# Kernel tuning notes

Hardware: AMD Instinct MI355X
Metric: run time of the kernel (lower is better)

Reference implementation:

```python
import jax, jax.numpy as jnp
import numpy as np

D_MODEL = 1024
STATE_DIM = 256


def setup_inputs() -> dict:
    key = jax.random.key(0)
    k_u, k_lam, k_B, k_C = jax.random.split(key, 4)
    u = jax.random.normal(k_u, (4, 4096, D_MODEL), dtype=jnp.float32)
    # log_lambda ~ N(3.0, 0.5^2), matching torch.randn(state_dim)*0.5 + 3.0
    log_lambda = jax.random.normal(k_lam, (STATE_DIM,), dtype=jnp.float32) * 0.5 + 3.0
    # torch Linear weights: B.weight [state_dim, d_model], C.weight [d_model, state_dim]
    B_w = jax.random.normal(k_B, (STATE_DIM, D_MODEL), dtype=jnp.float32) / np.sqrt(D_MODEL)
    C_w = jax.random.normal(k_C, (D_MODEL, STATE_DIM), dtype=jnp.float32) / np.sqrt(STATE_DIM)
    D = jnp.zeros((D_MODEL,), dtype=jnp.float32)
    return {"u": u, "log_lambda": log_lambda, "B_w": B_w, "C_w": C_w, "D": D}


def reference(u, log_lambda, B_w, C_w, D):
    # u: [batch, seq, d_model]
    lam = jax.nn.sigmoid(log_lambda)                      # [state_dim]
    Bu = jnp.einsum('bsd,nd->bsn', u, B_w)                # [batch, seq, state_dim]

    def step(h, bu_t):
        h = lam * h + bu_t                                # [batch, state_dim]
        return h, h

    h0 = jnp.zeros((u.shape[0], lam.shape[0]), dtype=u.dtype)
    # scan over time axis; Bu transposed to [seq, batch, state_dim]
    _, hs = jax.lax.scan(step, h0, jnp.swapaxes(Bu, 0, 1))
    hs = jnp.swapaxes(hs, 0, 1)                           # [batch, seq, state_dim]
    y = jnp.einsum('bsn,dn->bsd', hs, C_w) + D * u        # [batch, seq, d_model]
    return y
```

## Files before the change

### kernel.cpp

```cpp
#include <hip/hip_runtime.h>
#include <math.h>

typedef unsigned short ushort_t;
typedef __bf16 v8bf __attribute__((ext_vector_type(8)));
typedef __bf16 v4bf __attribute__((ext_vector_type(4)));
typedef float  v4f  __attribute__((ext_vector_type(4)));
typedef float  f32x4 __attribute__((ext_vector_type(4)));

#define BATCH 4
#define SEQ 4096
#define DM 1024
#define NS 256
#define MROWS (BATCH*SEQ)

#define NCH 128
#define CL (SEQ/NCH)

#define BK 32

typedef __attribute__((address_space(1))) void as1_void;
typedef __attribute__((address_space(3))) void as3_void;

__device__ __forceinline__ void gl_lds16(const void* g, void* l) {
    __builtin_amdgcn_global_load_lds((as1_void*)g, (as3_void*)l, 16, 0, 0);
}

__device__ __forceinline__ ushort_t f2bf(float f) {
    unsigned u = __builtin_bit_cast(unsigned, f);
    u += 0x7fff + ((u >> 16) & 1);
    return (ushort_t)(u >> 16);
}

__device__ __forceinline__ float sigm(float x) { return 1.0f / (1.0f + expf(-x)); }

__device__ __forceinline__ float powk(int e, float l1, float l2, float l4,
                                      float l8, float l16) {
    float w = 1.0f;
    if (e & 1)  w *= l1;
    if (e & 2)  w *= l2;
    if (e & 4)  w *= l4;
    if (e & 8)  w *= l8;
    if (e & 16) w *= l16;
    return w;
}

__global__ __launch_bounds__(256)
void gemm1_fused(const float* __restrict__ A,
                 const ushort_t* __restrict__ B,
                 float* __restrict__ Bu,
                 const float* __restrict__ ll,
                 float* __restrict__ cf)
{
    const int K = DM;
    __shared__ __align__(16) ushort_t As[2][128*BK];
    __shared__ __align__(16) ushort_t Bs[2][64*BK];

    const int tid  = threadIdx.x;
    const int lane = tid & 63;
    const int wave = tid >> 6;
    const int wrow = wave >> 1;
    const int wcol = wave & 1;
    const int n0 = blockIdx.x * 64;
    const int m0 = blockIdx.y * 128;

    const int fr = lane & 15;
    const int fq = lane >> 4;

    int arow[4], ac4[4];
    #pragma unroll
    for (int j = 0; j < 4; ++j) {
        int cid = j*256 + tid;
        arow[j] = cid >> 3;
        ac4[j]  = (cid & 7) * 4;
    }
    const int brow = tid >> 2;
    const int bcol = (tid & 3) * 8;

    f32x4 acc[4][2] = {};
    v4f areg[4];

    #pragma unroll
    for (int j = 0; j < 4; ++j)
        areg[j] = *(const v4f*)&A[(size_t)(m0 + arow[j])*K + ac4[j]];
    gl_lds16(&B[(size_t)(n0 + brow)*K + bcol], &Bs[0][tid*8]);

    for (int it = 0; it < K/BK; ++it) {
        const int cur = it & 1;
        #pragma unroll
        for (int j = 0; j < 4; ++j)
            *(v4bf*)&As[cur][arow[j]*BK + ac4[j]] = __builtin_convertvector(areg[j], v4bf);
        __syncthreads();

        if (it + 1 < K/BK) {
            const int k1 = (it + 1) * BK;
            gl_lds16(&B[(size_t)(n0 + brow)*K + k1 + bcol], &Bs[cur ^ 1][tid*8]);
            #pragma unroll
            for (int j = 0; j < 4; ++j)
                areg[j] = *(const v4f*)&A[(size_t)(m0 + arow[j])*K + k1 + ac4[j]];
        }

        v8bf af[4], bf[2];
        #pragma unroll
        for (int mi = 0; mi < 4; ++mi)
            af[mi] = *reinterpret_cast<const v8bf*>(&As[cur][(wrow*64 + mi*16 + fr)*BK + fq*8]);
        #pragma unroll
        for (int ni = 0; ni < 2; ++ni)
            bf[ni] = *reinterpret_cast<const v8bf*>(&Bs[cur][(wcol*32 + ni*16 + fr)*BK + fq*8]);

        #pragma unroll
        for (int mi = 0; mi < 4; ++mi)
            #pragma unroll
            for (int ni = 0; ni < 2; ++ni)
                acc[mi][ni] = __builtin_amdgcn_mfma_f32_16x16x32_bf16(
                                  af[mi], bf[ni], acc[mi][ni], 0, 0, 0);
    }

    const int orow = m0 + wrow*64 + (lane >> 4)*4;
    const int ocol = n0 + wcol*32 + (lane & 15);
    #pragma unroll
    for (int mi = 0; mi < 4; ++mi)
        #pragma unroll
        for (int ni = 0; ni < 2; ++ni)
            #pragma unroll
            for (int r = 0; r < 4; ++r)
                Bu[(size_t)(orow + mi*16 + r) * NS + (ocol + ni*16)] = acc[mi][ni][r];

    const int b_idx  = m0 >> 12;
    const int c_base = (m0 & 4095) >> 5;
    const int base   = (lane >> 4) * 4;

    #pragma unroll
    for (int ni = 0; ni < 2; ++ni) {
        const int col = ocol + ni*16;
        const float l1  = sigm(ll[col]);
        const float l2  = l1*l1;
        const float l4  = l2*l2;
        const float l8  = l4*l4;
        const float l16 = l8*l8;
        #pragma unroll
        for (int half = 0; half < 2; ++half) {
            float f = 0.0f;
            #pragma unroll
            for (int mi2 = 0; mi2 < 2; ++mi2) {
                const int mi = half*2 + mi2;
                float w = powk(28 - mi2*16 - base, l1, l2, l4, l8, l16);
                f = fmaf(w, acc[mi][ni][3], f);
                w *= l1; f = fmaf(w, acc[mi][ni][2], f);
                w *= l1; f = fmaf(w, acc[mi][ni][1], f);
                w *= l1; f = fmaf(w, acc[mi][ni][0], f);
            }
            f += __shfl_xor(f, 16, 64);
            f += __shfl_xor(f, 32, 64);
            if ((lane >> 4) == 0) {
                const int chunk = c_base + wrow*2 + half;
                cf[((size_t)b_idx*NCH + chunk)*NS + col] = f;
            }
        }
    }
}

__global__ __launch_bounds__(256)
void gemm2_mfma(const ushort_t* __restrict__ A,
                const ushort_t* __restrict__ B,
                float* __restrict__ C,
                const float* __restrict__ Dvec, const float* __restrict__ U)
{
    const int K = NS;
    const int N = DM;
    __shared__ __align__(16) ushort_t As[2][128*BK];
    __shared__ __align__(16) ushort_t Bs[2][128*BK];

    const int tid  = threadIdx.x;
    const int lane = tid & 63;
    const int wave = tid >> 6;
    const int wrow = wave >> 1;
    const int wcol = wave & 1;
    const int n0 = blockIdx.x * 128;
    const int m0 = blockIdx.y * 128;

    const int fr = lane & 15;
    const int fq = lane >> 4;

    f32x4 acc[4][4] = {};

    const int ch0 = wave*128 + lane;
    const int ch1 = ch0 + 64;
    const int r0 = ch0 >> 2, c0 = (ch0 & 3) * 8;
    const int r1 = ch1 >> 2, c1 = (ch1 & 3) * 8;

    gl_lds16(&A[(size_t)(m0 + r0)*K + c0], &As[0][ch0*8]);
    gl_lds16(&B[(size_t)(n0 + r0)*K + c0], &Bs[0][ch0*8]);
    gl_lds16(&A[(size_t)(m0 + r1)*K + c1], &As[0][ch1*8]);
    gl_lds16(&B[(size_t)(n0 + r1)*K + c1], &Bs[0][ch1*8]);

    for (int it = 0; it < K/BK; ++it) {
        const int cur = it & 1;
        __syncthreads();

        if (it + 1 < K/BK) {
            const int k1 = (it + 1) * BK;
            gl_lds16(&A[(size_t)(m0 + r0)*K + k1 + c0], &As[cur^1][ch0*8]);
            gl_lds16(&B[(size_t)(n0 + r0)*K + k1 + c0], &Bs[cur^1][ch0*8]);
            gl_lds16(&A[(size_t)(m0 + r1)*K + k1 + c1], &As[cur^1][ch1*8]);
            gl_lds16(&B[(size_t)(n0 + r1)*K + k1 + c1], &Bs[cur^1][ch1*8]);
        }

        v8bf af[4], bf[4];
        #pragma unroll
        for (int mi = 0; mi < 4; ++mi)
            af[mi] = *reinterpret_cast<const v8bf*>(&As[cur][(wrow*64 + mi*16 + fr)*BK + fq*8]);
        #pragma unroll
        for (int ni = 0; ni < 4; ++ni)
            bf[ni] = *reinterpret_cast<const v8bf*>(&Bs[cur][(wcol*64 + ni*16 + fr)*BK + fq*8]);

        #pragma unroll
        for (int mi = 0; mi < 4; ++mi)
            #pragma unroll
            for (int ni = 0; ni < 4; ++ni)
                acc[mi][ni] = __builtin_amdgcn_mfma_f32_16x16x32_bf16(
                                  af[mi], bf[ni], acc[mi][ni], 0, 0, 0);
    }

    const int orow = m0 + wrow*64 + (lane >> 4)*4;
    const int ocol = n0 + wcol*64 + (lane & 15);
    #pragma unroll
    for (int ni = 0; ni < 4; ++ni) {
        const int col = ocol + ni*16;
        const float d = Dvec[col];
        #pragma unroll
        for (int mi = 0; mi < 4; ++mi) {
            #pragma unroll
            for (int r = 0; r < 4; ++r) {
                const size_t idx = (size_t)(orow + mi*16 + r) * N + col;
                float v = acc[mi][ni][r];
                if (d != 0.0f) v = fmaf(d, U[idx], v);
                C[idx] = v;
            }
        }
    }
}

__global__ __launch_bounds__(256)
void cvt_w(const float4* __restrict__ Bw, const float4* __restrict__ Cw,
           ushort_t* __restrict__ Bo, ushort_t* __restrict__ Co)
{
    const int i = blockIdx.x * 256 + threadIdx.x;
    const float4* src = blockIdx.y ? Cw : Bw;
    ushort_t*     dst = blockIdx.y ? Co : Bo;
    float4 v = src[i];
    ushort4 o;
    o.x = f2bf(v.x); o.y = f2bf(v.y); o.z = f2bf(v.z); o.w = f2bf(v.w);
    *(ushort4*)&dst[4*(size_t)i] = o;
}

__global__ __launch_bounds__(256)
void carry_scan(const float* __restrict__ ll, const float* __restrict__ cf,
                float* __restrict__ carry)
{
    const int n = threadIdx.x, b = blockIdx.x;
    const float lam = sigm(ll[n]);
    float lamL = lam;
    #pragma unroll
    for (int i = 0; i < 5; ++i) lamL *= lamL;

    const float* cfb = cf    + (size_t)b*NCH*NS + n;
    float*       cab = carry + (size_t)b*NCH*NS + n;

    float x = 0.0f;
    for (int c0 = 0; c0 < NCH; c0 += 16) {
        float v[16];
        #pragma unroll
        for (int j = 0; j < 16; ++j) v[j] = cfb[(size_t)(c0 + j)*NS];
        #pragma unroll
        for (int j = 0; j < 16; ++j) {
            cab[(size_t)(c0 + j)*NS] = x;
            x = fmaf(lamL, x, v[j]);
        }
    }
}

__global__ __launch_bounds__(256)
void scan_apply(const float* __restrict__ Bu, const float* __restrict__ ll,
                const float* __restrict__ carry, ushort_t* __restrict__ hs16)
{
    const int n = threadIdx.x, c = blockIdx.x, b = blockIdx.y;
    const float lam = sigm(ll[n]);
    const size_t base = ((size_t)b*SEQ + (size_t)c*CL)*NS + n;

    float v[CL];
    #pragma unroll
    for (int t = 0; t < CL; ++t) v[t] = Bu[base + (size_t)t*NS];

    float h = carry[((size_t)b*NCH + c)*NS + n];
    #pragma unroll
    for (int t = 0; t < CL; ++t) { h = fmaf(lam, h, v[t]); v[t] = h; }
    #pragma unroll
    for (int t = 0; t < CL; ++t) hs16[base + (size_t)t*NS] = f2bf(v[t]);
}

extern "C" void kernel_launch(void* const* d_in, const int* in_sizes, int n_in,
                              void* d_out, int out_size, void* d_ws, size_t ws_size,
                              hipStream_t stream) {
    const float* u          = (const float*)d_in[0];
    const float* log_lambda = (const float*)d_in[1];
    const float* B_w        = (const float*)d_in[2];
    const float* C_w        = (const float*)d_in[3];
    const float* Dv         = (const float*)d_in[4];
    float* y  = (float*)d_out;

    char* w = (char*)d_ws;
    float*    Bu    = (float*)w;
    ushort_t* hs16  = (ushort_t*)(w + 16777216);
    ushort_t* Bw16  = (ushort_t*)(w + 25165824);
    ushort_t* Cw16  = (ushort_t*)(w + 25690112);
    float*    cf    = (float*)(w + 26214400);
    float*    carry = (float*)(w + 26738688);

    dim3 blk(256);

    cvt_w<<<dim3(256, 2), blk, 0, stream>>>((const float4*)B_w, (const float4*)C_w,
                                            Bw16, Cw16);

    gemm1_fused<<<dim3(NS/64, MROWS/128), blk, 0, stream>>>(
        u, Bw16, Bu, log_lambda, cf);

    carry_scan<<<dim3(BATCH),      blk, 0, stream>>>(log_lambda, cf, carry);
    scan_apply<<<dim3(NCH, BATCH), blk, 0, stream>>>(Bu, log_lambda, carry, hs16);

    gemm2_mfma<<<dim3(DM/128, MROWS/128), blk, 0, stream>>>(
        hs16, Cw16, y, Dv, u);
}
```

Baseline: 182.3 us.

## Split-K GEMM1 with full-N tiles so u is read once

GEMM1 now has each block own a 64-row M tile covering all 256 state columns, and the K dimension is split in two across blocks. Previously each u row was re-read and re-converted by four N-tile blocks. Each K-half writes partial Bu and chunk-carry buffers, and scan_apply and carry_scan sum the two partials. The cost is twice the Bu write and read traffic (fp32 partials of 16 MB each) and a larger workspace, in exchange for cutting the fp32 u reads from four passes to one.

```diff
diff --git a/kernel.cpp b/kernel.cpp
--- a/kernel.cpp
+++ b/kernel.cpp
@@ -17,6 +17,8 @@
 #define CL (SEQ/NCH)
 
 #define BK 32
+#define KSPLIT 2
+#define KHALF (DM/KSPLIT)
 
 typedef __attribute__((address_space(1))) void as1_void;
 typedef __attribute__((address_space(3))) void as3_void;
@@ -47,102 +49,113 @@
 __global__ __launch_bounds__(256)
 void gemm1_fused(const float* __restrict__ A,
                  const ushort_t* __restrict__ B,
-                 float* __restrict__ Bu,
+                 float* __restrict__ BuP,
                  const float* __restrict__ ll,
-                 float* __restrict__ cf)
+                 float* __restrict__ cfP)
 {
     const int K = DM;
-    __shared__ __align__(16) ushort_t As[2][128*BK];
-    __shared__ __align__(16) ushort_t Bs[2][64*BK];
+    __shared__ __align__(16) ushort_t As[2][64*BK];
+    __shared__ __align__(16) ushort_t Bs[2][256*BK];
 
     const int tid  = threadIdx.x;
     const int lane = tid & 63;
     const int wave = tid >> 6;
-    const int wrow = wave >> 1;
-    const int wcol = wave & 1;
-    const int n0 = blockIdx.x * 64;
-    const int m0 = blockIdx.y * 128;
+    const int kidx = blockIdx.x;
+    const int m0   = blockIdx.y * 64;
+    const int kb   = kidx * KHALF;
 
     const int fr = lane & 15;
     const int fq = lane >> 4;
 
-    int arow[4], ac4[4];
-    #pragma unroll
-    for (int j = 0; j < 4; ++j) {
+    int arow[2], ac4[2];
+    #pragma unroll
+    for (int j = 0; j < 2; ++j) {
         int cid = j*256 + tid;
         arow[j] = cid >> 3;
         ac4[j]  = (cid & 7) * 4;
     }
-    const int brow = tid >> 2;
-    const int bcol = (tid & 3) * 8;
-
-    f32x4 acc[4][2] = {};
-    v4f areg[4];
-
+    int brow[4], bc[4];
+    #pragma unroll
+    for (int j = 0; j < 4; ++j) {
+        int cid = j*256 + tid;
+        brow[j] = cid >> 2;
+        bc[j]   = (cid & 3) * 8;
+    }
+
+    f32x4 acc[4][4] = {};
+    v4f areg[2];
+
+    #pragma unroll
+    for (int j = 0; j < 2; ++j)
+        areg[j] = *(const v4f*)&A[(size_t)(m0 + arow[j])*K + kb + ac4[j]];
     #pragma unroll
     for (int j = 0; j < 4; ++j)
-        areg[j] = *(const v4f*)&A[(size_t)(m0 + arow[j])*K + ac4[j]];
-    gl_lds16(&B[(size_t)(n0 + brow)*K + bcol], &Bs[0][tid*8]);
-
-    for (int it = 0; it < K/BK; ++it) {
+        gl_lds16(&B[(size_t)brow[j]*K + kb + bc[j]], &Bs[0][(j*256 + tid)*8]);
+
+    for (int it = 0; it < KHALF/BK; ++it) {
         const int cur = it & 1;
         #pragma unroll
-        for (int j = 0; j < 4; ++j)
+        for (int j = 0; j < 2; ++j)
             *(v4bf*)&As[cur][arow[j]*BK + ac4[j]] = __builtin_convertvector(areg[j], v4bf);
         __syncthreads();
 
-        if (it + 1 < K/BK) {
-            const int k1 = (it + 1) * BK;
-            gl_lds16(&B[(size_t)(n0 + brow)*K + k1 + bcol], &Bs[cur ^ 1][tid*8]);
+        if (it + 1 < KHALF/BK) {
+            const int k1 = kb + (it + 1) * BK;
             #pragma unroll
             for (int j = 0; j < 4; ++j)
+                gl_lds16(&B[(size_t)brow[j]*K + k1 + bc[j]], &Bs[cur^1][(j*256 + tid)*8]);
+            #pragma unroll
+            for (int j = 0; j < 2; ++j)
                 areg[j] = *(const v4f*)&A[(size_t)(m0 + arow[j])*K + k1 + ac4[j]];
         }
 
-        v8bf af[4], bf[2];
+        v8bf af[4], bf[4];
         #pragma unroll
         for (int mi = 0; mi < 4; ++mi)
-            af[mi] = *reinterpret_cast<const v8bf*>(&As[cur][(wrow*64 + mi*16 + fr)*BK + fq*8]);
-        #pragma unroll
-        for (int ni = 0; ni < 2; ++ni)
-            bf[ni] = *reinterpret_cast<const v8bf*>(&Bs[cur][(wcol*32 + ni*16 + fr)*BK + fq*8]);
+            af[mi] = *reinterpret_cast<const v8bf*>(&As[cur][(mi*16 + fr)*BK + fq*8]);
+        #pragma unroll
+        for (int ni = 0; ni < 4; ++ni)
+            bf[ni] = *reinterpret_cast<const v8bf*>(&Bs[cur][(wave*64 + ni*16 + fr)*BK + fq*8]);
 
         #pragma unroll
         for (int mi = 0; mi < 4; ++mi)
             #pragma unroll
-            for (int ni = 0; ni < 2; ++ni)
+            for (int ni = 0; ni < 4; ++ni)
                 acc[mi][ni] = __builtin_amdgcn_mfma_f32_16x16x32_bf16(
                                   af[mi], bf[ni], acc[mi][ni], 0, 0, 0);
     }
 
-    const int orow = m0 + wrow*64 + (lane >> 4)*4;
-    const int ocol = n0 + wcol*32 + (lane & 15);
-    #pragma unroll
-    for (int mi = 0; mi < 4; ++mi)
-        #pragma unroll
-        for (int ni = 0; ni < 2; ++ni)
+    float* Bu = BuP + (size_t)kidx*MROWS*NS;
+    const int base = (lane >> 4) * 4;
+    #pragma unroll
+    for (int mi = 0; mi < 4; ++mi) {
+        #pragma unroll
+        for (int ni = 0; ni < 4; ++ni) {
+            const int col = wave*64 + ni*16 + fr;
             #pragma unroll
             for (int r = 0; r < 4; ++r)
-                Bu[(size_t)(orow + mi*16 + r) * NS + (ocol + ni*16)] = acc[mi][ni][r];
+                Bu[(size_t)(m0 + mi*16 + base + r)*NS + col] = acc[mi][ni][r];
+        }
+    }
 
     const int b_idx  = m0 >> 12;
     const int c_base = (m0 & 4095) >> 5;
-    const int base   = (lane >> 4) * 4;
-
-    #pragma unroll
-    for (int ni = 0; ni < 2; ++ni) {
-        const int col = ocol + ni*16;
+    float* cfk = cfP + (size_t)kidx*BATCH*NCH*NS;
+
+    #pragma unroll
+    for (int ni = 0; ni < 4; ++ni) {
+        const int col = wave*64 + ni*16 + fr;
         const float l1  = sigm(ll[col]);
         const float l2  = l1*l1;
         const float l4  = l2*l2;
         const float l8  = l4*l4;
         const float l16 = l8*l8;
         #pragma unroll
-        for (int half = 0; half < 2; ++half) {
+        for (int h = 0; h < 2; ++h) {
             float f = 0.0f;
             #pragma unroll
             for (int mi2 = 0; mi2 < 2; ++mi2) {
-                const int mi = half*2 + mi2;
+                const int mi = 2*h + mi2;
                 float w = powk(28 - mi2*16 - base, l1, l2, l4, l8, l16);
                 f = fmaf(w, acc[mi][ni][3], f);
                 w *= l1; f = fmaf(w, acc[mi][ni][2], f);
@@ -152,8 +165,8 @@
             f += __shfl_xor(f, 16, 64);
             f += __shfl_xor(f, 32, 64);
             if ((lane >> 4) == 0) {
-                const int chunk = c_base + wrow*2 + half;
-                cf[((size_t)b_idx*NCH + chunk)*NS + col] = f;
+                const int chunk = c_base + h;
+                cfk[((size_t)b_idx*NCH + chunk)*NS + col] = f;
             }
         }
     }
@@ -254,7 +267,7 @@
 }
 
 __global__ __launch_bounds__(256)
-void carry_scan(const float* __restrict__ ll, const float* __restrict__ cf,
+void carry_scan(const float* __restrict__ ll, const float* __restrict__ cfP,
                 float* __restrict__ carry)
 {
     const int n = threadIdx.x, b = blockIdx.x;
@@ -263,14 +276,16 @@
     #pragma unroll
     for (int i = 0; i < 5; ++i) lamL *= lamL;
 
-    const float* cfb = cf    + (size_t)b*NCH*NS + n;
+    const float* cf0 = cfP + (size_t)b*NCH*NS + n;
+    const float* cf1 = cf0 + (size_t)BATCH*NCH*NS;
     float*       cab = carry + (size_t)b*NCH*NS + n;
 
     float x = 0.0f;
     for (int c0 = 0; c0 < NCH; c0 += 16) {
         float v[16];
         #pragma unroll
-        for (int j = 0; j < 16; ++j) v[j] = cfb[(size_t)(c0 + j)*NS];
+        for (int j = 0; j < 16; ++j)
+            v[j] = cf0[(size_t)(c0 + j)*NS] + cf1[(size_t)(c0 + j)*NS];
         #pragma unroll
         for (int j = 0; j < 16; ++j) {
             cab[(size_t)(c0 + j)*NS] = x;
@@ -280,16 +295,19 @@
 }
 
 __global__ __launch_bounds__(256)
-void scan_apply(const float* __restrict__ Bu, const float* __restrict__ ll,
+void scan_apply(const float* __restrict__ BuP, const float* __restrict__ ll,
                 const float* __restrict__ carry, ushort_t* __restrict__ hs16)
 {
     const int n = threadIdx.x, c = blockIdx.x, b = blockIdx.y;
     const float lam = sigm(ll[n]);
     const size_t base = ((size_t)b*SEQ + (size_t)c*CL)*NS + n;
+    const float* Bu0 = BuP;
+    const float* Bu1 = BuP + (size_t)MROWS*NS;
 
     float v[CL];
     #pragma unroll
-    for (int t = 0; t < CL; ++t) v[t] = Bu[base + (size_t)t*NS];
+    for (int t = 0; t < CL; ++t)
+        v[t] = Bu0[base + (size_t)t*NS] + Bu1[base + (size_t)t*NS];
 
     float h = carry[((size_t)b*NCH + c)*NS + n];
     #pragma unroll
@@ -309,23 +327,23 @@
     float* y  = (float*)d_out;
 
     char* w = (char*)d_ws;
-    float*    Bu    = (float*)w;
-    ushort_t* hs16  = (ushort_t*)(w + 16777216);
-    ushort_t* Bw16  = (ushort_t*)(w + 25165824);
-    ushort_t* Cw16  = (ushort_t*)(w + 25690112);
-    float*    cf    = (float*)(w + 26214400);
-    float*    carry = (float*)(w + 26738688);
+    float*    BuP   = (float*)w;
+    ushort_t* hs16  = (ushort_t*)(w + 33554432);
+    ushort_t* Bw16  = (ushort_t*)(w + 41943040);
+    ushort_t* Cw16  = (ushort_t*)(w + 42467328);
+    float*    cfP   = (float*)(w + 42991616);
+    float*    carry = (float*)(w + 44040192);
 
     dim3 blk(256);
 
     cvt_w<<<dim3(256, 2), blk, 0, stream>>>((const float4*)B_w, (const float4*)C_w,
                                             Bw16, Cw16);
 
-    gemm1_fused<<<dim3(NS/64, MROWS/128), blk, 0, stream>>>(
-        u, Bw16, Bu, log_lambda, cf);
-
-    carry_scan<<<dim3(BATCH),      blk, 0, stream>>>(log_lambda, cf, carry);
-    scan_apply<<<dim3(NCH, BATCH), blk, 0, stream>>>(Bu, log_lambda, carry, hs16);
+    gemm1_fused<<<dim3(KSPLIT, MROWS/64), blk, 0, stream>>>(
+        u, Bw16, BuP, log_lambda, cfP);
+
+    carry_scan<<<dim3(BATCH),      blk, 0, stream>>>(log_lambda, cfP, carry);
+    scan_apply<<<dim3(NCH, BATCH), blk, 0, stream>>>(BuP, log_lambda, carry, hs16);
 
     gemm2_mfma<<<dim3(DM/128, MROWS/128), blk, 0, stream>>>(
         hs16, Cw16, y, Dv, u);
```

Measured after the change: 173.4 us. -4.9%, faster.
